# Kernel optimization log

Hardware: AMD Instinct MI355X
Metric: run time of the kernel (lower is better)

The kernel has to match this reference:

```python
import jax, jax.numpy as jnp
import numpy as np

NUM_EXPERTS = 8
TOP_K = 2
N_EMBD = 1024
D_FFN = 2048  # 4*n_embd//top_k, already multiple of block_size=128


def setup_inputs() -> dict:
    key = jax.random.key(0)
    k1, k2, k3, k4 = jax.random.split(key, 4)
    x = jax.random.normal(k1, (4, 2048, N_EMBD), dtype=jnp.float32)
    router_w = jax.random.normal(k2, (NUM_EXPERTS, N_EMBD), dtype=jnp.float32) * 0.02
    w1 = jax.random.normal(k3, (N_EMBD, D_FFN * NUM_EXPERTS), dtype=jnp.float32) * 0.02
    w2 = jax.random.normal(k4, (D_FFN * NUM_EXPERTS, N_EMBD), dtype=jnp.float32) * 0.02
    return {"x": x, "router_w": router_w, "w1": w1, "w2": w2}


def reference(x, router_w, w1, w2):
    B, T, D = x.shape
    xf = x.reshape(B * T, D)                       # [N, d]
    N = B * T

    # Router: softmax over experts, then top-k selection and renormalization.
    logits = xf @ router_w.T                       # [N, E]
    probs = jax.nn.softmax(logits, axis=-1)
    top_v, top_i = jax.lax.top_k(probs, TOP_K)     # [N, k]
    top_v = top_v / jnp.sum(top_v, axis=-1, keepdims=True)  # norm_topk_prob=True

    # Dense [N, E] routing-weight matrix (zero for non-selected experts).
    gate = jnp.zeros((N, NUM_EXPERTS), dtype=x.dtype)
    gate = gate.at[jnp.arange(N)[:, None], top_i].set(top_v)

    w1r = w1.reshape(D, NUM_EXPERTS, D_FFN)        # expert-major column blocks
    w2r = w2.reshape(NUM_EXPERTS, D_FFN, D)

    out = jnp.zeros((N, D), dtype=x.dtype)
    for e in range(NUM_EXPERTS):
        h = jax.nn.gelu(xf @ w1r[:, e, :], approximate=False)  # [N, f]
        out = out + gate[:, e:e + 1] * (h @ w2r[e])
    return out.reshape(B, T, D)
```

## Files before the change

kernel.cpp:

```cpp
#include <hip/hip_runtime.h>
#include <hip/hip_bf16.h>
#include <cstdint>
#include <cstddef>

#define NE 8
#define N_TOK 8192
#define D_EMB 1024
#define D_FFN 2048

#define BM 128
#define BN 128
#define BK 32

typedef __attribute__((ext_vector_type(8))) short short8;
typedef __attribute__((ext_vector_type(4))) float f32x4;

__device__ __forceinline__ unsigned short f2bf(float f) {
  union { float f; unsigned int u; } c; c.f = f;
  unsigned int u = c.u;
  unsigned int r = u + 0x7FFFu + ((u >> 16) & 1u);
  return (unsigned short)(r >> 16);
}

__device__ __forceinline__ float bf2f(unsigned short u) {
  union { unsigned int u; float f; } c; c.u = ((unsigned int)u) << 16;
  return c.f;
}

__device__ __forceinline__ float gelu_f(float x) {
  float u = x * x * x * 0.044715f + x;
  float t = __expf(-1.5957691216057308f * u);
  return x * __builtin_amdgcn_rcpf(1.f + t);
}

__device__ __forceinline__ void gll16(const void* g, void* l) {
  __builtin_amdgcn_global_load_lds((const __attribute__((address_space(1))) void*)g,
                                   (__attribute__((address_space(3))) void*)l, 16, 0, 0);
}

#define SB() __builtin_amdgcn_sched_barrier(0)
#define VW(N) { asm volatile("s_waitcnt vmcnt(" #N ")" ::: "memory"); SB(); }
#define BAR() { SB(); __builtin_amdgcn_s_barrier(); SB(); }

__global__ __launch_bounds__(256) void router_k(const float* __restrict__ x,
                                                const float* __restrict__ rw,
                                                int* __restrict__ ti,
                                                float* __restrict__ tg,
                                                ushort* __restrict__ xb) {
  int w = threadIdx.x >> 6, lane = threadIdx.x & 63;
  int n = blockIdx.x * 4 + w;
  const float4* x4 = (const float4*)(x + (size_t)n * D_EMB);
  ushort4* xb4 = (ushort4*)(xb + (size_t)n * D_EMB);
  const float4* r4 = (const float4*)rw;
  float acc[NE];
#pragma unroll
  for (int e = 0; e < NE; ++e) acc[e] = 0.f;
#pragma unroll
  for (int c = 0; c < 4; ++c) {
    float4 xv = x4[c * 64 + lane];
    ushort4 o;
    o.x = f2bf(xv.x); o.y = f2bf(xv.y); o.z = f2bf(xv.z); o.w = f2bf(xv.w);
    xb4[c * 64 + lane] = o;
#pragma unroll
    for (int e = 0; e < NE; ++e) {
      float4 wv = r4[e * 256 + c * 64 + lane];
      acc[e] += xv.x * wv.x + xv.y * wv.y + xv.z * wv.z + xv.w * wv.w;
    }
  }
#pragma unroll
  for (int e = 0; e < NE; ++e) {
    float v = acc[e];
#pragma unroll
    for (int off = 32; off >= 1; off >>= 1) v += __shfl_xor(v, off);
    acc[e] = v;
  }
  if (lane == 0) {
    int e0 = 0; float v0 = acc[0];
#pragma unroll
    for (int e = 1; e < NE; ++e) if (acc[e] > v0) { v0 = acc[e]; e0 = e; }
    int e1 = -1; float v1 = -1e30f;
#pragma unroll
    for (int e = 0; e < NE; ++e) if (e != e0 && acc[e] > v1) { v1 = acc[e]; e1 = e; }
    float p1 = expf(v1 - v0);
    float g0 = 1.f / (1.f + p1);
    float g1 = p1 * g0;
    ti[2 * n] = e0; ti[2 * n + 1] = e1;
    tg[2 * n] = g0; tg[2 * n + 1] = g1;
  }
}

__global__ __launch_bounds__(256) void hist_k(const int* __restrict__ ti,
                                              int* __restrict__ counts) {
  __shared__ int lc[NE];
  if (threadIdx.x < NE) lc[threadIdx.x] = 0;
  __syncthreads();
  int s = blockIdx.x * 512 + threadIdx.x;
  atomicAdd(&lc[ti[s]], 1);
  atomicAdd(&lc[ti[s + 256]], 1);
  __syncthreads();
  if (threadIdx.x < NE) atomicAdd(&counts[threadIdx.x], lc[threadIdx.x]);
}

__global__ void prefix_k(const int* __restrict__ counts, int* __restrict__ bases,
                         int* __restrict__ cursor) {
  if (threadIdx.x == 0) {
    int s = 0;
    for (int e = 0; e < NE; ++e) { bases[e] = s; cursor[e] = s; s += counts[e]; }
  }
}

__global__ __launch_bounds__(256) void scatter_k(const int* __restrict__ ti,
                                                 const float* __restrict__ tg,
                                                 int* __restrict__ cursor,
                                                 int* __restrict__ tokS,
                                                 float* __restrict__ gate) {
  __shared__ int lc[NE], lb[NE];
  if (threadIdx.x < NE) lc[threadIdx.x] = 0;
  __syncthreads();
  int s = blockIdx.x * 256 + threadIdx.x;
  int e = ti[s];
  float g = tg[s];
  int loc = atomicAdd(&lc[e], 1);
  __syncthreads();
  if (threadIdx.x < NE) lb[threadIdx.x] = atomicAdd(&cursor[threadIdx.x], lc[threadIdx.x]);
  __syncthreads();
  int pos = lb[e] + loc;
  tokS[pos] = s;
  gate[pos] = g;
}

__global__ __launch_bounds__(256) void transpose_bf_k(const float* __restrict__ src,
                                                      ushort* __restrict__ dst,
                                                      int R, int C) {
  __shared__ ushort t[32][33];
  int bx = blockIdx.x, by = blockIdx.y;
  int rl = threadIdx.x >> 3, q = threadIdx.x & 7;
  float4 v = *(const float4*)&src[(size_t)(by * 32 + rl) * C + bx * 32 + q * 4];
  t[rl][q * 4 + 0] = f2bf(v.x);
  t[rl][q * 4 + 1] = f2bf(v.y);
  t[rl][q * 4 + 2] = f2bf(v.z);
  t[rl][q * 4 + 3] = f2bf(v.w);
  __syncthreads();
  ushort4 o;
  o.x = t[q * 4 + 0][rl];
  o.y = t[q * 4 + 1][rl];
  o.z = t[q * 4 + 2][rl];
  o.w = t[q * 4 + 3][rl];
  *(ushort4*)&dst[(size_t)(bx * 32 + rl) * R + by * 32 + q * 4] = o;
}


#define STG(BUF)                                                           \
  { _Pragma("unroll") for (int j_ = 0; j_ < 2; ++j_) {                     \
      gll16(aptr[j_], &Al[BUF][ldso[j_]]);                                 \
      gll16(bptr[j_], &Bl[BUF][ldso[j_]]);                                 \
      aptr[j_] += BK; bptr[j_] += BK;                                      \
    } }

#define CMP(BUF)                                                           \
  { short8 a[4], b[4];                                                     \
    _Pragma("unroll") for (int i_ = 0; i_ < 4; ++i_)                       \
      a[i_] = *(const short8*)&Al[BUF][arow + i_ * 16 * BK];               \
    _Pragma("unroll") for (int j_ = 0; j_ < 4; ++j_)                       \
      b[j_] = *(const short8*)&Bl[BUF][brow + j_ * 16 * BK];               \
    _Pragma("unroll") for (int i_ = 0; i_ < 4; ++i_)                       \
      _Pragma("unroll") for (int j_ = 0; j_ < 4; ++j_)                     \
        acc[i_][j_] = __builtin_amdgcn_mfma_f32_16x16x32_bf16(a[i_], b[j_], acc[i_][j_], 0, 0, 0); \
  }

#define KLOOP(NT)                                                          \
  STG(0);                                                                  \
  for (int ks = 0; ks < (NT) - 2; ks += 2) {                               \
    STG(1); VW(4); BAR(); CMP(0); BAR();                                   \
    STG(0); VW(4); BAR(); CMP(1); BAR();                                   \
  }                                                                        \
  STG(1); VW(4); BAR(); CMP(0); BAR();                                     \
  VW(0); BAR(); CMP(1);

__global__ __launch_bounds__(256) void gemm1_k(const ushort* __restrict__ xb,
                                               const ushort* __restrict__ w1t,
                                               const int* __restrict__ counts,
                                               const int* __restrict__ bases,
                                               const int* __restrict__ tokS,
                                               ushort* __restrict__ h) {
  int bid = (int)blockIdx.x;
  bid = (bid & 7) * (NE * 1024 / 8) + (bid >> 3);
  int e = bid >> 10;
  int rem = bid & 1023;
  int mt = rem >> 4, nt = rem & 15;
  int count = counts[e];
  if (mt * BM >= count) return;
  int base = bases[e];

  __shared__ ushort Al[2][BM * BK];
  __shared__ ushort Bl[2][BN * BK];

  int tid = threadIdx.x;
  int w = tid >> 6, lane = tid & 63;

  const int ssw = (((lane & 3) ^ ((lane >> 3) & 3))) * 8;

  const ushort* aptr[2]; const ushort* bptr[2];
  int ldso[2];
#pragma unroll
  for (int j = 0; j < 2; ++j) {
    int rl = w * 32 + j * 16 + (lane >> 2);
    int pr = min(base + mt * BM + rl, base + count - 1);
    int t = tokS[pr] >> 1;
    aptr[j] = xb + (size_t)t * D_EMB + ssw;
    int c = e * D_FFN + nt * BN + rl;
    bptr[j] = w1t + (size_t)c * D_EMB + ssw;
    ldso[j] = (w * 32 + j * 16) * BK;
  }

  f32x4 zero = {0.f, 0.f, 0.f, 0.f};
  f32x4 acc[4][4];
#pragma unroll
  for (int i = 0; i < 4; ++i)
#pragma unroll
    for (int j = 0; j < 4; ++j) acc[i][j] = zero;

  int wm = w >> 1, wn = w & 1;
  const int rsw = ((lane >> 4) ^ (((lane & 15) >> 1) & 3)) * 8;
  const int arow = (wm * 64 + (lane & 15)) * BK + rsw;
  const int brow = (wn * 64 + (lane & 15)) * BK + rsw;

  KLOOP(D_EMB / BK);

  int r0 = mt * BM + wm * 64, c0 = nt * BN + wn * 64;
#pragma unroll
  for (int i = 0; i < 4; ++i) {
#pragma unroll
    for (int q = 0; q < 4; ++q) {
      int row = r0 + i * 16 + (lane >> 4) * 4 + q;
      if (row < count) {
        size_t hb = (size_t)(base + row) * D_FFN;
#pragma unroll
        for (int j = 0; j < 4; ++j) {
          h[hb + c0 + j * 16 + (lane & 15)] = f2bf(gelu_f(acc[i][j][q]));
        }
      }
    }
  }
}

__global__ __launch_bounds__(256) void gemm2_k(const ushort* __restrict__ h,
                                               const ushort* __restrict__ w2t,
                                               const int* __restrict__ counts,
                                               const int* __restrict__ bases,
                                               const int* __restrict__ tokS,
                                               const float* __restrict__ gate,
                                               ushort* __restrict__ y2) {
  int bid = (int)blockIdx.x;
  bid = (bid & 7) * (NE * 512 / 8) + (bid >> 3);
  int e = bid >> 9;
  int rem = bid & 511;
  int mt = rem >> 3, nt = rem & 7;
  int count = counts[e];
  if (mt * BM >= count) return;
  int base = bases[e];

  __shared__ ushort Al[2][BM * BK];
  __shared__ ushort Bl[2][BN * BK];

  int tid = threadIdx.x;
  int w = tid >> 6, lane = tid & 63;

  const int ssw = (((lane & 3) ^ ((lane >> 3) & 3))) * 8;

  const ushort* aptr[2]; const ushort* bptr[2];
  int ldso[2];
#pragma unroll
  for (int j = 0; j < 2; ++j) {
    int rl = w * 32 + j * 16 + (lane >> 2);
    int pr = min(base + mt * BM + rl, base + count - 1);
    aptr[j] = h + (size_t)pr * D_FFN + ssw;
    int d = nt * BN + rl;
    bptr[j] = w2t + (size_t)d * (NE * D_FFN) + e * D_FFN + ssw;
    ldso[j] = (w * 32 + j * 16) * BK;
  }

  f32x4 zero = {0.f, 0.f, 0.f, 0.f};
  f32x4 acc[4][4];
#pragma unroll
  for (int i = 0; i < 4; ++i)
#pragma unroll
    for (int j = 0; j < 4; ++j) acc[i][j] = zero;

  int wm = w >> 1, wn = w & 1;
  const int rsw = ((lane >> 4) ^ (((lane & 15) >> 1) & 3)) * 8;
  const int arow = (wm * 64 + (lane & 15)) * BK + rsw;
  const int brow = (wn * 64 + (lane & 15)) * BK + rsw;

  KLOOP(D_FFN / BK);

  int r0 = mt * BM + wm * 64, c0 = nt * BN + wn * 64;
#pragma unroll
  for (int i = 0; i < 4; ++i) {
#pragma unroll
    for (int q = 0; q < 4; ++q) {
      int row = r0 + i * 16 + (lane >> 4) * 4 + q;
      if (row < count) {
        int pr = base + row;
        float g = gate[pr];
        size_t yb = (size_t)tokS[pr] * D_EMB;
#pragma unroll
        for (int j = 0; j < 4; ++j) {
          y2[yb + c0 + j * 16 + (lane & 15)] = f2bf(g * acc[i][j][q]);
        }
      }
    }
  }
}

__global__ __launch_bounds__(256) void combine_k(const ushort* __restrict__ y2,
                                                 float* __restrict__ out) {
  int n = blockIdx.x;
  const ushort4* r0 = (const ushort4*)(y2 + (size_t)(2 * n) * D_EMB);
  const ushort4* r1 = (const ushort4*)(y2 + (size_t)(2 * n + 1) * D_EMB);
  float4* o = (float4*)(out + (size_t)n * D_EMB);
  int i = threadIdx.x;
  ushort4 a = r0[i], b = r1[i];
  float4 v;
  v.x = bf2f(a.x) + bf2f(b.x);
  v.y = bf2f(a.y) + bf2f(b.y);
  v.z = bf2f(a.z) + bf2f(b.z);
  v.w = bf2f(a.w) + bf2f(b.w);
  o[i] = v;
}

extern "C" void kernel_launch(void* const* d_in, const int* in_sizes, int n_in,
                              void* d_out, int out_size, void* d_ws, size_t ws_size,
                              hipStream_t stream) {
  const float* x  = (const float*)d_in[0];
  const float* rw = (const float*)d_in[1];
  const float* w1 = (const float*)d_in[2];
  const float* w2 = (const float*)d_in[3];
  float* out = (float*)d_out;

  char* ws = (char*)d_ws;
  size_t off = 0;
  auto alloc = [&](size_t bytes) {
    void* p = ws + off;
    off = (off + bytes + 255) & ~(size_t)255;
    return p;
  };
  int*    counts = (int*)alloc(32);
  int*    bases  = (int*)alloc(32);
  int*    cursor = (int*)alloc(32);
  int*    ti     = (int*)alloc((size_t)N_TOK * 2 * sizeof(int));
  float*  tg     = (float*)alloc((size_t)N_TOK * 2 * sizeof(float));
  int*    tokS   = (int*)alloc((size_t)N_TOK * 2 * sizeof(int));
  float*  gate   = (float*)alloc((size_t)N_TOK * 2 * sizeof(float));
  ushort* xb     = (ushort*)alloc((size_t)N_TOK * D_EMB * 2);
  ushort* w1t    = (ushort*)alloc((size_t)D_EMB * NE * D_FFN * 2);
  ushort* w2t    = (ushort*)alloc((size_t)D_EMB * NE * D_FFN * 2);
  ushort* hbuf   = (ushort*)alloc((size_t)N_TOK * 2 * D_FFN * 2);
  ushort* ybuf   = (ushort*)alloc((size_t)N_TOK * 2 * D_EMB * 2);
  (void)ws_size; (void)in_sizes; (void)n_in; (void)out_size;

  hipMemsetAsync(counts, 0, 32, stream);

  router_k<<<N_TOK / 4, 256, 0, stream>>>(x, rw, ti, tg, xb);
  transpose_bf_k<<<dim3(512, 32), 256, 0, stream>>>(w1, w1t, D_EMB, NE * D_FFN);
  transpose_bf_k<<<dim3(32, 512), 256, 0, stream>>>(w2, w2t, NE * D_FFN, D_EMB);
  hist_k<<<N_TOK * 2 / 512, 256, 0, stream>>>(ti, counts);
  prefix_k<<<1, 64, 0, stream>>>(counts, bases, cursor);
  scatter_k<<<N_TOK * 2 / 256, 256, 0, stream>>>(ti, tg, cursor, tokS, gate);
  gemm1_k<<<NE * 64 * 16, 256, 0, stream>>>(xb, w1t, counts, bases, tokS, hbuf);
  gemm2_k<<<NE * 64 * 8, 256, 0, stream>>>(hbuf, w2t, counts, bases, tokS, gate, ybuf);
  combine_k<<<N_TOK, 256, 0, stream>>>(ybuf, out);
}
```

Before: 281.8 us.

## Triple-buffer gemm1 k-loop and store w2 transpose in expert-major layout

gemm1 moves from a double-buffered to a triple-buffered LDS pipeline, prefetching two k-tiles ahead to hide global load latency. The w2 transpose now writes a per-expert contiguous [E][D][F] layout, and gemm2 indexes it accordingly. The extra LDS buffer raises shared memory per block, which may lower occupancy.

```diff
diff --git a/kernel.cpp b/kernel.cpp
--- a/kernel.cpp
+++ b/kernel.cpp
@@ -149,6 +149,28 @@
   *(ushort4*)&dst[(size_t)(bx * 32 + rl) * R + by * 32 + q * 4] = o;
 }
 
+__global__ __launch_bounds__(256) void transpose_w2e_k(const float* __restrict__ src,
+                                                       ushort* __restrict__ dst) {
+  __shared__ ushort t[32][33];
+  int bx = blockIdx.x, by = blockIdx.y;
+  int rl = threadIdx.x >> 3, q = threadIdx.x & 7;
+  float4 v = *(const float4*)&src[(size_t)(by * 32 + rl) * D_EMB + bx * 32 + q * 4];
+  t[rl][q * 4 + 0] = f2bf(v.x);
+  t[rl][q * 4 + 1] = f2bf(v.y);
+  t[rl][q * 4 + 2] = f2bf(v.z);
+  t[rl][q * 4 + 3] = f2bf(v.w);
+  __syncthreads();
+  int e = by >> 6;
+  int f0 = (by & 63) * 32;
+  size_t eoff = (size_t)e * (D_EMB * D_FFN);
+  ushort4 o;
+  o.x = t[q * 4 + 0][rl];
+  o.y = t[q * 4 + 1][rl];
+  o.z = t[q * 4 + 2][rl];
+  o.w = t[q * 4 + 3][rl];
+  *(ushort4*)&dst[eoff + (size_t)(bx * 32 + rl) * D_FFN + f0 + q * 4] = o;
+}
+
 
 #define STG(BUF)                                                           \
   { _Pragma("unroll") for (int j_ = 0; j_ < 2; ++j_) {                     \
@@ -175,6 +197,16 @@
     STG(0); VW(4); BAR(); CMP(1); BAR();                                   \
   }                                                                        \
   STG(1); VW(4); BAR(); CMP(0); BAR();                                     \
+  VW(0); BAR(); CMP(1);
+
+#define KLOOP3(NT)                                                         \
+  STG(0); STG(1);                                                          \
+  for (int ks = 0; ks < (NT) - 2; ks += 3) {                               \
+    STG(2); VW(8); BAR(); CMP(0); BAR();                                   \
+    STG(0); VW(8); BAR(); CMP(1); BAR();                                   \
+    STG(1); VW(8); BAR(); CMP(2); BAR();                                   \
+  }                                                                        \
+  VW(4); BAR(); CMP(0); BAR();                                             \
   VW(0); BAR(); CMP(1);
 
 __global__ __launch_bounds__(256) void gemm1_k(const ushort* __restrict__ xb,
@@ -192,8 +224,8 @@
   if (mt * BM >= count) return;
   int base = bases[e];
 
-  __shared__ ushort Al[2][BM * BK];
-  __shared__ ushort Bl[2][BN * BK];
+  __shared__ ushort Al[3][BM * BK];
+  __shared__ ushort Bl[3][BN * BK];
 
   int tid = threadIdx.x;
   int w = tid >> 6, lane = tid & 63;
@@ -225,7 +257,7 @@
   const int arow = (wm * 64 + (lane & 15)) * BK + rsw;
   const int brow = (wn * 64 + (lane & 15)) * BK + rsw;
 
-  KLOOP(D_EMB / BK);
+  KLOOP3(D_EMB / BK);
 
   int r0 = mt * BM + wm * 64, c0 = nt * BN + wn * 64;
 #pragma unroll
@@ -245,7 +277,7 @@
 }
 
 __global__ __launch_bounds__(256) void gemm2_k(const ushort* __restrict__ h,
-                                               const ushort* __restrict__ w2t,
+                                               const ushort* __restrict__ w2te,
                                                const int* __restrict__ counts,
                                                const int* __restrict__ bases,
                                                const int* __restrict__ tokS,
@@ -276,7 +308,7 @@
     int pr = min(base + mt * BM + rl, base + count - 1);
     aptr[j] = h + (size_t)pr * D_FFN + ssw;
     int d = nt * BN + rl;
-    bptr[j] = w2t + (size_t)d * (NE * D_FFN) + e * D_FFN + ssw;
+    bptr[j] = w2te + (size_t)e * (D_EMB * D_FFN) + (size_t)d * D_FFN + ssw;
     ldso[j] = (w * 32 + j * 16) * BK;
   }
 
@@ -354,7 +386,7 @@
   float*  gate   = (float*)alloc((size_t)N_TOK * 2 * sizeof(float));
   ushort* xb     = (ushort*)alloc((size_t)N_TOK * D_EMB * 2);
   ushort* w1t    = (ushort*)alloc((size_t)D_EMB * NE * D_FFN * 2);
-  ushort* w2t    = (ushort*)alloc((size_t)D_EMB * NE * D_FFN * 2);
+  ushort* w2te   = (ushort*)alloc((size_t)D_EMB * NE * D_FFN * 2);
   ushort* hbuf   = (ushort*)alloc((size_t)N_TOK * 2 * D_FFN * 2);
   ushort* ybuf   = (ushort*)alloc((size_t)N_TOK * 2 * D_EMB * 2);
   (void)ws_size; (void)in_sizes; (void)n_in; (void)out_size;
@@ -363,11 +395,11 @@
 
   router_k<<<N_TOK / 4, 256, 0, stream>>>(x, rw, ti, tg, xb);
   transpose_bf_k<<<dim3(512, 32), 256, 0, stream>>>(w1, w1t, D_EMB, NE * D_FFN);
-  transpose_bf_k<<<dim3(32, 512), 256, 0, stream>>>(w2, w2t, NE * D_FFN, D_EMB);
+  transpose_w2e_k<<<dim3(32, 512), 256, 0, stream>>>(w2, w2te);
   hist_k<<<N_TOK * 2 / 512, 256, 0, stream>>>(ti, counts);
   prefix_k<<<1, 64, 0, stream>>>(counts, bases, cursor);
   scatter_k<<<N_TOK * 2 / 256, 256, 0, stream>>>(ti, tg, cursor, tokS, gate);
   gemm1_k<<<NE * 64 * 16, 256, 0, stream>>>(xb, w1t, counts, bases, tokS, hbuf);
-  gemm2_k<<<NE * 64 * 8, 256, 0, stream>>>(hbuf, w2t, counts, bases, tokS, gate, ybuf);
+  gemm2_k<<<NE * 64 * 8, 256, 0, stream>>>(hbuf, w2te, counts, bases, tokS, gate, ybuf);
   combine_k<<<N_TOK, 256, 0, stream>>>(ybuf, out);
 }
```

Measured after the change: 307.6 us. 9.1% more time.
